# Kernel optimization log

Measured on AMD Instinct MI355X. Metric: run time of the kernel, lower is better.

The kernel has to match this reference:

```python
import jax, jax.numpy as jnp
import numpy as np

B, T, V, D, H, C = 64, 512, 50000, 128, 256, 50


def setup_inputs() -> dict:
    key = jax.random.key(0)
    ks = jax.random.split(key, 15)
    s = 0.05
    rn = lambda k, shape: jax.random.normal(k, shape, jnp.float32) * s
    words = jax.random.randint(ks[0], (B, T), 0, V)
    target = jax.random.randint(ks[1], (B, T), 0, C)
    seq_len = jax.random.randint(ks[2], (B,), T // 2, T + 1)
    seq_len = seq_len.at[0].set(T)  # ensure at least one full-length sequence
    return dict(
        words=words, target=target, seq_len=seq_len,
        emb=rn(ks[3], (V, D)),
        W_ih_f=rn(ks[4], (4 * H, D)), W_hh_f=rn(ks[5], (4 * H, H)), b_f=rn(ks[6], (4 * H,)),
        W_ih_b=rn(ks[7], (4 * H, D)), W_hh_b=rn(ks[8], (4 * H, H)), b_b=rn(ks[9], (4 * H,)),
        fc_W=rn(ks[10], (C, 2 * H)), fc_b=rn(ks[11], (C,)),
        trans=rn(ks[12], (C, C)), start_s=rn(ks[13], (C,)), end_s=rn(ks[14], (C,)),
    )


def _lstm(x, W_ih, W_hh, b):
    # unidirectional LSTM, PyTorch gate order (i, f, g, o). x: [B,T,D] -> h: [B,T,H]
    Hh = W_hh.shape[1]
    xg = jnp.einsum('btd,gd->btg', x, W_ih) + b  # [B,T,4H]

    def step(carry, xt):
        h, c = carry
        g = xt + h @ W_hh.T
        i, f, gg, o = jnp.split(g, 4, axis=-1)
        c = jax.nn.sigmoid(f) * c + jax.nn.sigmoid(i) * jnp.tanh(gg)
        h = jax.nn.sigmoid(o) * jnp.tanh(c)
        return (h, c), h

    h0 = jnp.zeros((x.shape[0], Hh), x.dtype)
    _, hs = jax.lax.scan(step, (h0, h0), jnp.swapaxes(xg, 0, 1))
    return jnp.swapaxes(hs, 0, 1)


def _rev_idx(seq_len, t_len):
    # per-sequence time-reversal indices (packed-sequence semantics for the backward LSTM)
    t = jnp.arange(t_len)[None, :]
    L = seq_len[:, None]
    return jnp.where(t < L, L - 1 - t, t)


def _bilstm_crf_loss(words, target, seq_len, emb, W_ih_f, W_hh_f, b_f,
                     W_ih_b, W_hh_b, b_b, fc_W, fc_b, trans, start_s, end_s):
    x = emb[words]  # [B,T,D]
    h_f = _lstm(x, W_ih_f, W_hh_f, b_f)
    idx = _rev_idx(seq_len, x.shape[1])
    x_rev = jnp.take_along_axis(x, idx[:, :, None], axis=1)
    h_b = jnp.take_along_axis(_lstm(x_rev, W_ih_b, W_hh_b, b_b), idx[:, :, None], axis=1)
    feats = jnp.concatenate([h_f, h_b], axis=-1) @ fc_W.T + fc_b  # [B,T,C]
    logits = jax.nn.log_softmax(feats, axis=-1)
    mask = jnp.arange(x.shape[1])[None, :] < seq_len[:, None]  # [B,T] bool

    # --- CRF normalizer (forward algorithm) ---
    alpha0 = logits[:, 0] + start_s  # [B,C]

    def step(alpha, inp):
        emit_t, m_t = inp  # [B,C], [B]
        tmp = alpha[:, :, None] + trans[None, :, :] + emit_t[:, None, :]
        new = jax.nn.logsumexp(tmp, axis=1)
        return jnp.where(m_t[:, None], new, alpha), None

    alpha, _ = jax.lax.scan(step, alpha0,
                            (jnp.swapaxes(logits, 0, 1)[1:], jnp.swapaxes(mask, 0, 1)[1:]))
    norm = jax.nn.logsumexp(alpha + end_s, axis=1)  # [B]

    # --- gold path score ---
    maskf = mask.astype(logits.dtype)
    emit = jnp.take_along_axis(logits, target[:, :, None], axis=2)[..., 0]  # [B,T]
    trans_sc = trans[target[:, :-1], target[:, 1:]]  # [B,T-1]
    last = target[jnp.arange(target.shape[0]), seq_len - 1]
    gold = (emit * maskf).sum(1) + (trans_sc * maskf[:, 1:]).sum(1) \
           + start_s[target[:, 0]] + end_s[last]

    return jnp.mean(norm - gold)


def reference(words, target, seq_len, emb, W_ih_f, W_hh_f, b_f,
              W_ih_b, W_hh_b, b_b, fc_W, fc_b, trans, start_s, end_s):
    return _bilstm_crf_loss(words, target, seq_len, emb, W_ih_f, W_hh_f, b_f,
                            W_ih_b, W_hh_b, b_b, fc_W, fc_b, trans, start_s, end_s)
```

## Files before the change

### kernel.cpp

```cpp
#include <hip/hip_runtime.h>
#include <hip/hip_bf16.h>

#define BB 64
#define TT 512
#define DD 128
#define HH 256
#define G4 1024
#define CC 50

typedef __bf16 bf16x8 __attribute__((ext_vector_type(8)));
typedef float  f32x4  __attribute__((ext_vector_type(4)));
typedef _Float16 h16x2 __attribute__((ext_vector_type(2)));

#if defined(__has_builtin)
#if __has_builtin(__builtin_amdgcn_fdot2)
#define HAS_FDOT2 1
#endif
#endif

__device__ __forceinline__ float bl16(unsigned u) { return __uint_as_float(u << 16); }
__device__ __forceinline__ float bh16(unsigned u) { return __uint_as_float(u & 0xffff0000u); }

__device__ __forceinline__ float sigf(float x) {
    return 1.f / (1.f + __expf(-x));
}
__device__ __forceinline__ float tanh_s(float x) {
    float ax = fabsf(x);
    float e = __expf(-2.f * ax);
    float r = (1.f - e) / (1.f + e);
    return copysignf(r, x);
}

__device__ __forceinline__ float dot8(float acc, uint4 w, uint4 h) {
#ifdef HAS_FDOT2
    acc = __builtin_amdgcn_fdot2(__builtin_bit_cast(h16x2, w.x),
                                 __builtin_bit_cast(h16x2, h.x), acc, false);
    acc = __builtin_amdgcn_fdot2(__builtin_bit_cast(h16x2, w.y),
                                 __builtin_bit_cast(h16x2, h.y), acc, false);
    acc = __builtin_amdgcn_fdot2(__builtin_bit_cast(h16x2, w.z),
                                 __builtin_bit_cast(h16x2, h.z), acc, false);
    acc = __builtin_amdgcn_fdot2(__builtin_bit_cast(h16x2, w.w),
                                 __builtin_bit_cast(h16x2, h.w), acc, false);
#else
    {
        h16x2 a = __builtin_bit_cast(h16x2, w.x), b = __builtin_bit_cast(h16x2, h.x);
        acc = fmaf((float)a.x, (float)b.x, acc); acc = fmaf((float)a.y, (float)b.y, acc);
        a = __builtin_bit_cast(h16x2, w.y); b = __builtin_bit_cast(h16x2, h.y);
        acc = fmaf((float)a.x, (float)b.x, acc); acc = fmaf((float)a.y, (float)b.y, acc);
        a = __builtin_bit_cast(h16x2, w.z); b = __builtin_bit_cast(h16x2, h.z);
        acc = fmaf((float)a.x, (float)b.x, acc); acc = fmaf((float)a.y, (float)b.y, acc);
        a = __builtin_bit_cast(h16x2, w.w); b = __builtin_bit_cast(h16x2, h.w);
        acc = fmaf((float)a.x, (float)b.x, acc); acc = fmaf((float)a.y, (float)b.y, acc);
    }
#endif
    return acc;
}

__global__ __launch_bounds__(256) void k_cvt(
    const float* __restrict__ src, __hip_bfloat16* __restrict__ dst, int n)
{
    int i = (blockIdx.x * 256 + threadIdx.x) * 8;
    if (i + 8 <= n) {
        float4 a = *(const float4*)(src + i);
        float4 b = *(const float4*)(src + i + 4);
        __hip_bfloat16 o[8];
        o[0] = __float2bfloat16(a.x); o[1] = __float2bfloat16(a.y);
        o[2] = __float2bfloat16(a.z); o[3] = __float2bfloat16(a.w);
        o[4] = __float2bfloat16(b.x); o[5] = __float2bfloat16(b.y);
        o[6] = __float2bfloat16(b.z); o[7] = __float2bfloat16(b.w);
        *(uint4*)(dst + i) = *(const uint4*)o;
    }
}

__global__ __launch_bounds__(256) void k_pack(
    const float* __restrict__ Wf, const float* __restrict__ Wb,
    uint4* __restrict__ Wp)
{
    int blk = blockIdx.x;
    int g   = blk & 3;
    int kc  = (blk >> 2) & 31;
    int dir = blk >> 7;
    int j = threadIdx.x;
    int row = g * 256 + j;
    const float* src = (dir ? Wb : Wf) + (size_t)row * 256 + kc * 8;
    float4 a = *(const float4*)src;
    float4 b = *(const float4*)(src + 4);
    _Float16 o[8];
    o[0] = (_Float16)a.x; o[1] = (_Float16)a.y;
    o[2] = (_Float16)a.z; o[3] = (_Float16)a.w;
    o[4] = (_Float16)b.x; o[5] = (_Float16)b.y;
    o[6] = (_Float16)b.z; o[7] = (_Float16)b.w;
    Wp[((size_t)(dir * 32 + kc) * 4 + g) * 256 + j] = *(const uint4*)o;
}

__global__ __launch_bounds__(256, 2) void k_xg(
    const int* __restrict__ words,
    const float* __restrict__ embf,
    const __hip_bfloat16* __restrict__ Wih,
    const float* __restrict__ bfv, const float* __restrict__ bbv,
    __hip_bfloat16* __restrict__ xg)
{
    __shared__ __align__(16) __hip_bfloat16 A[64][136];
    int tid = threadIdx.x;
    int bt0 = blockIdx.x * 64;

    {
        int r = tid >> 2;
        int c0 = (tid & 3) * 32;
        int word = words[bt0 + r];
        const float* src = embf + (size_t)word * DD + c0;
#pragma unroll
        for (int i = 0; i < 8; ++i) {
            float4 v = *(const float4*)(src + i * 4);
            __hip_bfloat16 o[4] = {__float2bfloat16(v.x), __float2bfloat16(v.y),
                                   __float2bfloat16(v.z), __float2bfloat16(v.w)};
            *(uint2*)&A[r][c0 + i * 4] = *(const uint2*)o;
        }
    }
    __syncthreads();

    int wave = tid >> 6, lane = tid & 63;
    int m = lane & 15, quad = lane >> 4;

    bf16x8 afr[4][4];
#pragma unroll
    for (int ms = 0; ms < 4; ++ms)
#pragma unroll
        for (int kf = 0; kf < 4; ++kf)
            afr[ms][kf] = *(const bf16x8*)&A[ms * 16 + m][quad * 8 + kf * 32];

#pragma unroll 1
    for (int i = 0; i < 32; ++i) {
        int nt = wave * 32 + i;
        int gate_g = nt * 16 + m;
        int dir = gate_g >> 10;
        int gate = gate_g & 1023;
        const __hip_bfloat16* brow = Wih + (size_t)gate_g * DD + quad * 8;
        bf16x8 bfr[4];
#pragma unroll
        for (int kf = 0; kf < 4; ++kf) bfr[kf] = *(const bf16x8*)(brow + kf * 32);
        float bv = dir ? bbv[gate] : bfv[gate];
        size_t dbase = (size_t)dir * (size_t)(BB * TT * G4);

#pragma unroll
        for (int ms = 0; ms < 4; ++ms) {
            f32x4 acc = {0.f, 0.f, 0.f, 0.f};
#pragma unroll
            for (int kf = 0; kf < 4; ++kf)
                acc = __builtin_amdgcn_mfma_f32_16x16x32_bf16(afr[ms][kf], bfr[kf], acc, 0, 0, 0);
#pragma unroll
            for (int r = 0; r < 4; ++r) {
                int btrow = bt0 + ms * 16 + quad * 4 + r;
                xg[dbase + (size_t)btrow * G4 + gate] = __float2bfloat16(acc[r] + bv);
            }
        }
    }
}

__global__ __launch_bounds__(512)
__attribute__((amdgpu_waves_per_eu(2, 2)))
void k_lstm(
    const __hip_bfloat16* __restrict__ xg,
    const uint4* __restrict__ Wp,
    const int* __restrict__ seq_len,
    __hip_bfloat16* __restrict__ hcat)
{
    int b = blockIdx.x & 63;
    int dir = blockIdx.x >> 6;
    int tid = threadIdx.x;
    int j   = tid & 255;
    int half = tid >> 8;

    __shared__ __align__(16) uint4 wlds[16 * 512];
    __shared__ __align__(16) _Float16 hbf[2][HH];
    __shared__ float pbuf[4][HH];

    const uint4* Wd = Wp + (size_t)dir * (32 * 4 * 256);

    uint4 wr[12][4];
#pragma unroll
    for (int kcl = 0; kcl < 12; ++kcl)
#pragma unroll
        for (int g = 0; g < 4; ++g)
            wr[kcl][g] = Wd[(((kcl + 16 * half) * 4 + g) * 256) + j];

#pragma unroll
    for (int kcl = 12; kcl < 16; ++kcl)
#pragma unroll
        for (int g = 0; g < 4; ++g)
            wlds[((kcl - 12) * 4 + g) * 512 + tid] =
                Wd[(((kcl + 16 * half) * 4 + g) * 256) + j];

    if (half == 0) hbf[0][j] = (_Float16)0.f;
    float c = 0.f;
    int L = seq_len[b];
    const __hip_bfloat16* xgb = xg + (size_t)dir * (size_t)(BB * TT * G4)
                                   + (size_t)b * TT * G4;

    int tc = dir ? (L - 1) : 0;
    float xv0 = 0.f, xv1 = 0.f, xv2 = 0.f, xv3 = 0.f;
    if (half == 0) {
        const __hip_bfloat16* xr = xgb + (size_t)tc * G4 + j;
        xv0 = __bfloat162float(xr[0]);   xv1 = __bfloat162float(xr[256]);
        xv2 = __bfloat162float(xr[512]); xv3 = __bfloat162float(xr[768]);
    }
    __syncthreads();

#pragma unroll 1
    for (int t = 0; t < L; ++t) {
#pragma unroll
        for (int kcl = 0; kcl < 12; ++kcl)
#pragma unroll
            for (int g = 0; g < 4; ++g)
                asm volatile("" : "+v"(wr[kcl][g].x), "+v"(wr[kcl][g].y),
                                  "+v"(wr[kcl][g].z), "+v"(wr[kcl][g].w));

        int cur = t & 1, nxt = cur ^ 1;
        int tn = t + 1;
        int tcn = dir ? ((tn < L) ? (L - 1 - tn) : tn) : tn;
        bool pf = (tn < L);
        __hip_bfloat16 p0, p1, p2, p3;
        if (half == 0 && pf) {
            const __hip_bfloat16* xr = xgb + (size_t)tcn * G4 + j;
            p0 = xr[0]; p1 = xr[256]; p2 = xr[512]; p3 = xr[768];
        }

        unsigned off = 0;
        asm volatile("" : "+v"(off));

        const _Float16* hrow = &hbf[cur][half * 128];
        float a0 = 0.f, a1 = 0.f, a2 = 0.f, a3 = 0.f;
#pragma unroll
        for (int kcl = 0; kcl < 12; ++kcl) {
            uint4 hv = *(const uint4*)(hrow + kcl * 8);
            a0 = dot8(a0, wr[kcl][0], hv);
            a1 = dot8(a1, wr[kcl][1], hv);
            a2 = dot8(a2, wr[kcl][2], hv);
            a3 = dot8(a3, wr[kcl][3], hv);
        }
#pragma unroll
        for (int kcl = 12; kcl < 16; ++kcl) {
            uint4 hv = *(const uint4*)(hrow + kcl * 8);
            int m0 = (kcl - 12) * 4;
            uint4 w0 = wlds[(m0 + 0) * 512 + tid + off];
            uint4 w1 = wlds[(m0 + 1) * 512 + tid + off];
            uint4 w2 = wlds[(m0 + 2) * 512 + tid + off];
            uint4 w3 = wlds[(m0 + 3) * 512 + tid + off];
            a0 = dot8(a0, w0, hv);
            a1 = dot8(a1, w1, hv);
            a2 = dot8(a2, w2, hv);
            a3 = dot8(a3, w3, hv);
            __builtin_amdgcn_sched_barrier(0);
        }

        if (half) {
            pbuf[0][j] = a0; pbuf[1][j] = a1;
            pbuf[2][j] = a2; pbuf[3][j] = a3;
        }
        __syncthreads();

        if (half == 0) {
            float gi = a0 + pbuf[0][j] + xv0;
            float gf = a1 + pbuf[1][j] + xv1;
            float gg = a2 + pbuf[2][j] + xv2;
            float go = a3 + pbuf[3][j] + xv3;
            float i_ = sigf(gi), f_ = sigf(gf), G = tanh_s(gg), o_ = sigf(go);
            c = f_ * c + i_ * G;
            float h = o_ * tanh_s(c);
            hbf[nxt][j] = (_Float16)h;
            hcat[((size_t)(b * TT + tc)) * (2 * HH) + dir * HH + j] = __float2bfloat16(h);
            if (pf) {
                xv0 = __bfloat162float(p0); xv1 = __bfloat162float(p1);
                xv2 = __bfloat162float(p2); xv3 = __bfloat162float(p3);
            }
        }
        tc = tcn;
        __syncthreads();
    }
}

__global__ __launch_bounds__(256) void k_fc(
    const __hip_bfloat16* __restrict__ hcat,
    const __hip_bfloat16* __restrict__ fcW,
    const float* __restrict__ fcb,
    float* __restrict__ logits)
{
    int team = threadIdx.x >> 6;
    int tid  = threadIdx.x & 63;
    int row  = blockIdx.x * 4 + team;
    __shared__ __align__(16) float hrow[4][2 * HH];
    __shared__ float fbuf[4][CC + 2];

    {
        uint4 v = *(const uint4*)(hcat + (size_t)row * (2 * HH) + tid * 8);
        float* d = &hrow[team][tid * 8];
        d[0] = bl16(v.x); d[1] = bh16(v.x);
        d[2] = bl16(v.y); d[3] = bh16(v.y);
        d[4] = bl16(v.z); d[5] = bh16(v.z);
        d[6] = bl16(v.w); d[7] = bh16(v.w);
    }
    __syncthreads();

    if (tid < CC) {
        float acc = fcb[tid];
        const uint4* wr = (const uint4*)(fcW + (size_t)tid * (2 * HH));
#pragma unroll 8
        for (int kc = 0; kc < 64; ++kc) {
            uint4 wv = wr[kc];
            float4 h0 = *(const float4*)&hrow[team][kc * 8];
            float4 h1 = *(const float4*)&hrow[team][kc * 8 + 4];
            acc = fmaf(bl16(wv.x), h0.x, acc); acc = fmaf(bh16(wv.x), h0.y, acc);
            acc = fmaf(bl16(wv.y), h0.z, acc); acc = fmaf(bh16(wv.y), h0.w, acc);
            acc = fmaf(bl16(wv.z), h1.x, acc); acc = fmaf(bh16(wv.z), h1.y, acc);
            acc = fmaf(bl16(wv.w), h1.z, acc); acc = fmaf(bh16(wv.w), h1.w, acc);
        }
        fbuf[team][tid] = acc;
    }
    __syncthreads();

    float m = -1e30f;
    for (int i = 0; i < CC; ++i) m = fmaxf(m, fbuf[team][i]);
    float s = 0.f;
    for (int i = 0; i < CC; ++i) s += __expf(fbuf[team][i] - m);
    float lns = __logf(s);
    if (tid < CC) logits[(size_t)row * CC + tid] = fbuf[team][tid] - m - lns;
}

__global__ __launch_bounds__(256) void k_crf(
    const float* __restrict__ logits,
    const int* __restrict__ target,
    const int* __restrict__ seq_len,
    const float* __restrict__ trans,
    const float* __restrict__ start_s,
    const float* __restrict__ end_s,
    float* __restrict__ loss_b)
{
    const float L2E = 1.4426950408889634f;
    const float LN2 = 0.6931471805599453f;
    int b = blockIdx.x;
    int tid = threadIdx.x;
    int q = tid >> 6;
    int j = tid & 63;
    bool act = (j < CC);
    int L = seq_len[b];
    const float* lg = logits + (size_t)b * TT * CC;

    __shared__ float alpha2[64];
    __shared__ float mpart[4][64];
    __shared__ float spart[4][64];
    __shared__ float red[256];
    __shared__ float nbuf[CC + 2];

    int i0 = q * 13;
    int icnt = min(13, CC - i0);
    float treg[13];
    if (act) {
#pragma unroll
        for (int s = 0; s < 13; ++s)
            if (s < icnt) treg[s] = L2E * trans[(i0 + s) * CC + j];
    }
    if (q == 0 && act) alpha2[j] = L2E * (lg[j] + start_s[j]);
    __syncthreads();

    float v[13];
    float lgreg = 0.f;
    if (q == 0 && act) lgreg = lg[CC + j];
    for (int t = 1; t < L; ++t) {
        float lgnext = 0.f;
        if (q == 0 && act && (t + 1) < L)
            lgnext = lg[(size_t)(t + 1) * CC + j];

        float mq = -1e30f;
        if (act) {
#pragma unroll
            for (int s = 0; s < 13; ++s)
                if (s < icnt) { v[s] = alpha2[i0 + s] + treg[s]; mq = fmaxf(mq, v[s]); }
        }
        mpart[q][j] = mq;
        __syncthreads();
        float M = fmaxf(fmaxf(mpart[0][j], mpart[1][j]), fmaxf(mpart[2][j], mpart[3][j]));
        float sq = 0.f;
        if (act) {
#pragma unroll
            for (int s = 0; s < 13; ++s)
                if (s < icnt) sq += exp2f(v[s] - M);
        }
        spart[q][j] = sq;
        __syncthreads();
        if (q == 0 && act) {
            float S = spart[0][j] + spart[1][j] + spart[2][j] + spart[3][j];
            alpha2[j] = M + log2f(S) + L2E * lgreg;
        }
        lgreg = lgnext;
        __syncthreads();
    }

    if (q == 0 && act) nbuf[j] = alpha2[j] + L2E * end_s[j];

    float gp = 0.f;
    const int* tg = target + b * TT;
    for (int t = tid; t < TT; t += 256) {
        if (t < L) {
            int c = tg[t];
            gp += lg[(size_t)t * CC + c];
            if (t >= 1) gp += trans[tg[t - 1] * CC + c];
        }
    }
    red[tid] = gp;
    __syncthreads();

    if (tid == 0) {
        float m2 = -1e30f;
        for (int i = 0; i < CC; ++i) m2 = fmaxf(m2, nbuf[i]);
        float s2 = 0.f;
        for (int i = 0; i < CC; ++i) s2 += exp2f(nbuf[i] - m2);
        float norm_nat = (m2 + log2f(s2)) * LN2;
        float g = 0.f;
        for (int i = 0; i < 256; ++i) g += red[i];
        g += start_s[tg[0]] + end_s[tg[L - 1]];
        loss_b[b] = norm_nat - g;
    }
}

__global__ void k_fin(const float* __restrict__ loss_b, float* __restrict__ out)
{
    int t = threadIdx.x;
    float v = loss_b[t];
#pragma unroll
    for (int o = 32; o > 0; o >>= 1) v += __shfl_down(v, o);
    if (t == 0) out[0] = v * (1.f / BB);
}

extern "C" void kernel_launch(void* const* d_in, const int* in_sizes, int n_in,
                              void* d_out, int out_size, void* d_ws, size_t ws_size,
                              hipStream_t stream)
{
    const int* words   = (const int*)d_in[0];
    const int* target  = (const int*)d_in[1];
    const int* seq_len = (const int*)d_in[2];
    const float* emb    = (const float*)d_in[3];
    const float* W_ih_f = (const float*)d_in[4];
    const float* W_hh_f = (const float*)d_in[5];
    const float* b_f    = (const float*)d_in[6];
    const float* W_ih_b = (const float*)d_in[7];
    const float* W_hh_b = (const float*)d_in[8];
    const float* b_b    = (const float*)d_in[9];
    const float* fc_W   = (const float*)d_in[10];
    const float* fc_b   = (const float*)d_in[11];
    const float* trans  = (const float*)d_in[12];
    const float* start_s= (const float*)d_in[13];
    const float* end_s  = (const float*)d_in[14];

    char* ws = (char*)d_ws;
    __hip_bfloat16* xg     = (__hip_bfloat16*)ws;
    __hip_bfloat16* hcat   = (__hip_bfloat16*)(ws + 134217728);
    float*          logits = (float*)(ws + 167772160);
    uint4*          Wp     = (uint4*)(ws + 167772160);
    float*          loss_b = (float*)(ws + 174325760);
    __hip_bfloat16* wihall = (__hip_bfloat16*)(ws + 174326016);
    __hip_bfloat16* fcw_bf = (__hip_bfloat16*)(ws + 174850304);

    k_cvt<<<64,  256, 0, stream>>>(W_ih_f, wihall,          131072);
    k_cvt<<<64,  256, 0, stream>>>(W_ih_b, wihall + 131072, 131072);
    k_cvt<<<13,  256, 0, stream>>>(fc_W,   fcw_bf,          25600);
    k_pack<<<256, 256, 0, stream>>>(W_hh_f, W_hh_b, Wp);

    k_xg  <<<512, 256, 0, stream>>>(words, emb, wihall, b_f, b_b, xg);
    k_lstm<<<128, 512, 0, stream>>>(xg, Wp, seq_len, hcat);
    k_fc  <<<8192, 256, 0, stream>>>(hcat, fcw_bf, fc_b, logits);
    k_crf <<<64, 256, 0, stream>>>(logits, target, seq_len, trans, start_s, end_s, loss_b);
    k_fin <<<1, 64, 0, stream>>>(loss_b, (float*)d_out);
}
```

Baseline: 1.702 ms.

## Split LSTM recurrence across four thread groups, stream weights from cache

The recurrent LSTM kernel now runs 1024 threads per block instead of 512. The hidden-size reduction is split four ways, with partial sums combined through shared memory. Weights are no longer pinned in registers. Three quarters of each thread's weight chunks are reloaded from global memory (L1/L2) every timestep, and the remaining quarter sits in LDS. The aim is more parallelism per serial timestep and less register pressure, at the cost of global weight traffic every step and a larger partial-sum reduction.

Measured after the change: 2.636 ms. 54.9% more time.

```diff
diff --git a/kernel.cpp b/kernel.cpp
--- a/kernel.cpp
+++ b/kernel.cpp
@@ -157,8 +157,8 @@
     }
 }
 
-__global__ __launch_bounds__(512)
-__attribute__((amdgpu_waves_per_eu(2, 2)))
+__global__ __launch_bounds__(1024)
+__attribute__((amdgpu_waves_per_eu(4, 4)))
 void k_lstm(
     const __hip_bfloat16* __restrict__ xg,
     const uint4* __restrict__ Wp,
@@ -169,37 +169,30 @@
     int dir = blockIdx.x >> 6;
     int tid = threadIdx.x;
     int j   = tid & 255;
-    int half = tid >> 8;
-
-    __shared__ __align__(16) uint4 wlds[16 * 512];
+    int q   = tid >> 8;
+
+    __shared__ __align__(16) uint4 wlds[8 * 1024];
     __shared__ __align__(16) _Float16 hbf[2][HH];
-    __shared__ float pbuf[4][HH];
+    __shared__ float pbuf[3][4][HH];
 
     const uint4* Wd = Wp + (size_t)dir * (32 * 4 * 256);
-
-    uint4 wr[12][4];
-#pragma unroll
-    for (int kcl = 0; kcl < 12; ++kcl)
+    const uint4* Ws = Wd + (size_t)(q * 8) * 4 * 256 + j;
+
+#pragma unroll
+    for (int c = 6; c < 8; ++c)
 #pragma unroll
         for (int g = 0; g < 4; ++g)
-            wr[kcl][g] = Wd[(((kcl + 16 * half) * 4 + g) * 256) + j];
-
-#pragma unroll
-    for (int kcl = 12; kcl < 16; ++kcl)
-#pragma unroll
-        for (int g = 0; g < 4; ++g)
-            wlds[((kcl - 12) * 4 + g) * 512 + tid] =
-                Wd[(((kcl + 16 * half) * 4 + g) * 256) + j];
-
-    if (half == 0) hbf[0][j] = (_Float16)0.f;
-    float c = 0.f;
+            wlds[((c - 6) * 4 + g) * 1024 + tid] = Ws[(c * 4 + g) * 256];
+
+    if (q == 0) hbf[0][j] = (_Float16)0.f;
+    float cc = 0.f;
     int L = seq_len[b];
     const __hip_bfloat16* xgb = xg + (size_t)dir * (size_t)(BB * TT * G4)
                                    + (size_t)b * TT * G4;
 
     int tc = dir ? (L - 1) : 0;
     float xv0 = 0.f, xv1 = 0.f, xv2 = 0.f, xv3 = 0.f;
-    if (half == 0) {
+    if (q == 0) {
         const __hip_bfloat16* xr = xgb + (size_t)tc * G4 + j;
         xv0 = __bfloat162float(xr[0]);   xv1 = __bfloat162float(xr[256]);
         xv2 = __bfloat162float(xr[512]); xv3 = __bfloat162float(xr[768]);
@@ -208,65 +201,63 @@
 
 #pragma unroll 1
     for (int t = 0; t < L; ++t) {
-#pragma unroll
-        for (int kcl = 0; kcl < 12; ++kcl)
-#pragma unroll
-            for (int g = 0; g < 4; ++g)
-                asm volatile("" : "+v"(wr[kcl][g].x), "+v"(wr[kcl][g].y),
-                                  "+v"(wr[kcl][g].z), "+v"(wr[kcl][g].w));
-
         int cur = t & 1, nxt = cur ^ 1;
         int tn = t + 1;
         int tcn = dir ? ((tn < L) ? (L - 1 - tn) : tn) : tn;
         bool pf = (tn < L);
         __hip_bfloat16 p0, p1, p2, p3;
-        if (half == 0 && pf) {
+        if (q == 0 && pf) {
             const __hip_bfloat16* xr = xgb + (size_t)tcn * G4 + j;
             p0 = xr[0]; p1 = xr[256]; p2 = xr[512]; p3 = xr[768];
         }
 
-        unsigned off = 0;
-        asm volatile("" : "+v"(off));
-
-        const _Float16* hrow = &hbf[cur][half * 128];
+        unsigned off = 0, soff = 0;
+        asm volatile("" : "+v"(off), "+v"(soff));
+        const uint4* Wst = (const uint4*)((const char*)Ws + soff);
+
+        const _Float16* hrow = &hbf[cur][q * 64];
         float a0 = 0.f, a1 = 0.f, a2 = 0.f, a3 = 0.f;
-#pragma unroll
-        for (int kcl = 0; kcl < 12; ++kcl) {
-            uint4 hv = *(const uint4*)(hrow + kcl * 8);
-            a0 = dot8(a0, wr[kcl][0], hv);
-            a1 = dot8(a1, wr[kcl][1], hv);
-            a2 = dot8(a2, wr[kcl][2], hv);
-            a3 = dot8(a3, wr[kcl][3], hv);
-        }
-#pragma unroll
-        for (int kcl = 12; kcl < 16; ++kcl) {
-            uint4 hv = *(const uint4*)(hrow + kcl * 8);
-            int m0 = (kcl - 12) * 4;
-            uint4 w0 = wlds[(m0 + 0) * 512 + tid + off];
-            uint4 w1 = wlds[(m0 + 1) * 512 + tid + off];
-            uint4 w2 = wlds[(m0 + 2) * 512 + tid + off];
-            uint4 w3 = wlds[(m0 + 3) * 512 + tid + off];
+
+#pragma unroll
+        for (int c = 0; c < 6; ++c) {
+            uint4 hv = *(const uint4*)(hrow + c * 8);
+            uint4 w0 = Wst[(c * 4 + 0) * 256];
+            uint4 w1 = Wst[(c * 4 + 1) * 256];
+            uint4 w2 = Wst[(c * 4 + 2) * 256];
+            uint4 w3 = Wst[(c * 4 + 3) * 256];
             a0 = dot8(a0, w0, hv);
             a1 = dot8(a1, w1, hv);
             a2 = dot8(a2, w2, hv);
             a3 = dot8(a3, w3, hv);
-            __builtin_amdgcn_sched_barrier(0);
-        }
-
-        if (half) {
-            pbuf[0][j] = a0; pbuf[1][j] = a1;
-            pbuf[2][j] = a2; pbuf[3][j] = a3;
+        }
+#pragma unroll
+        for (int c = 6; c < 8; ++c) {
+            uint4 hv = *(const uint4*)(hrow + c * 8);
+            int m0 = (c - 6) * 4;
+            uint4 w0 = wlds[(m0 + 0) * 1024 + tid + off];
+            uint4 w1 = wlds[(m0 + 1) * 1024 + tid + off];
+            uint4 w2 = wlds[(m0 + 2) * 1024 + tid + off];
+            uint4 w3 = wlds[(m0 + 3) * 1024 + tid + off];
+            a0 = dot8(a0, w0, hv);
+            a1 = dot8(a1, w1, hv);
+            a2 = dot8(a2, w2, hv);
+            a3 = dot8(a3, w3, hv);
+        }
+
+        if (q) {
+            pbuf[q - 1][0][j] = a0; pbuf[q - 1][1][j] = a1;
+            pbuf[q - 1][2][j] = a2; pbuf[q - 1][3][j] = a3;
         }
         __syncthreads();
 
-        if (half == 0) {
-            float gi = a0 + pbuf[0][j] + xv0;
-            float gf = a1 + pbuf[1][j] + xv1;
-            float gg = a2 + pbuf[2][j] + xv2;
-            float go = a3 + pbuf[3][j] + xv3;
+        if (q == 0) {
+            float gi = a0 + pbuf[0][0][j] + pbuf[1][0][j] + pbuf[2][0][j] + xv0;
+            float gf = a1 + pbuf[0][1][j] + pbuf[1][1][j] + pbuf[2][1][j] + xv1;
+            float gg = a2 + pbuf[0][2][j] + pbuf[1][2][j] + pbuf[2][2][j] + xv2;
+            float go = a3 + pbuf[0][3][j] + pbuf[1][3][j] + pbuf[2][3][j] + xv3;
             float i_ = sigf(gi), f_ = sigf(gf), G = tanh_s(gg), o_ = sigf(go);
-            c = f_ * c + i_ * G;
-            float h = o_ * tanh_s(c);
+            cc = f_ * cc + i_ * G;
+            float h = o_ * tanh_s(cc);
             hbf[nxt][j] = (_Float16)h;
             hcat[((size_t)(b * TT + tc)) * (2 * HH) + dir * HH + j] = __float2bfloat16(h);
             if (pf) {
@@ -466,7 +457,7 @@
     k_pack<<<256, 256, 0, stream>>>(W_hh_f, W_hh_b, Wp);
 
     k_xg  <<<512, 256, 0, stream>>>(words, emb, wihall, b_f, b_b, xg);
-    k_lstm<<<128, 512, 0, stream>>>(xg, Wp, seq_len, hcat);
+    k_lstm<<<128, 1024, 0, stream>>>(xg, Wp, seq_len, hcat);
     k_fc  <<<8192, 256, 0, stream>>>(hcat, fcw_bf, fc_b, logits);
     k_crf <<<64, 256, 0, stream>>>(logits, target, seq_len, trans, start_s, end_s, loss_b);
     k_fin <<<1, 64, 0, stream>>>(loss_b, (float*)d_out);
```
